# Optimization experiments

Measured on AMD Instinct MI355X. Metric: run time of the kernel, lower is better.

## Reference

```python
import jax, jax.numpy as jnp
import numpy as np

N_NODES = 100000
N_EDGES = 1600000
IN_F = 128
HEADS = 4
D_K = 32
OUT_TOTAL = HEADS * D_K


def setup_inputs() -> dict:
    key = jax.random.key(0)
    k1, k2, k3, k4, k5, k6 = jax.random.split(key, 6)
    x = jax.random.normal(k1, (N_NODES, IN_F), dtype=jnp.float32)
    edge_index = jax.random.randint(k2, (2, N_EDGES), 0, N_NODES, dtype=jnp.int64)
    # torch nn.Linear weights: [out, in], xavier-uniform init
    def xavier(k, shape):
        fan_out, fan_in = shape
        lim = float(np.sqrt(6.0 / (fan_in + fan_out)))
        return jax.random.uniform(k, shape, dtype=jnp.float32, minval=-lim, maxval=lim)
    Wq = xavier(k3, (OUT_TOTAL, IN_F))
    Wk = xavier(k4, (OUT_TOTAL, IN_F))
    Wv = xavier(k5, (OUT_TOTAL, IN_F))
    # D init_type='uniform': U(-1, 1)
    D = jax.random.uniform(k6, (HEADS, D_K), dtype=jnp.float32, minval=-1.0, maxval=1.0)
    return {"x": x, "Wq": Wq, "Wk": Wk, "Wv": Wv, "D": D, "edge_index": edge_index}


def reference(x, Wq, Wk, Wv, D, edge_index):
    N = x.shape[0]
    scale = 1.0 / np.sqrt(D_K)
    Q = (x @ Wq.T).reshape(N, HEADS, D_K)
    K = (x @ Wk.T).reshape(N, HEADS, D_K)
    V = (x @ Wv.T).reshape(N, HEADS, D_K)
    row, col = edge_index[0], edge_index[1]
    K_i = K[row]              # [E, H, d]
    Q_j = Q[col]              # [E, H, d]
    diff = K_i - Q_j
    # non-self edges: diff^T diag(D) diff ; self edges: K^T diag(D) Q
    score_edge = jnp.sum(diff * D * diff, axis=-1)          # [E, H]
    score_self = jnp.sum(K_i * D * Q[row], axis=-1)         # [E, H]
    self_mask = (row == col)[:, None]
    scores = jnp.where(self_mask, score_self, score_edge)
    scores = jax.nn.leaky_relu(scores * scale, 0.2)
    # segment softmax over destination node `row`
    smax = jax.ops.segment_max(scores, row, num_segments=N)  # [N, H]
    ex = jnp.exp(scores - smax[row])
    ssum = jax.ops.segment_sum(ex, row, num_segments=N)      # [N, H]
    alpha = ex / (ssum[row] + 1e-16)
    # scatter-add aggregate alpha * V[col] into destination rows
    out = jax.ops.segment_sum(alpha[:, :, None] * V[col], row, num_segments=N)
    return out.reshape(N, OUT_TOTAL)
```

## Files before the change

### kernel.cpp

```cpp
#include <hip/hip_runtime.h>
#include <hip/hip_fp16.h>
#include <cmath>


#define HEADS 4
#define DK 32
#define FDIM 128
#define BINSHIFT 8
#define BINCAP 6144

typedef _Float16 f16x8 __attribute__((ext_vector_type(8)));
typedef float f32x4 __attribute__((ext_vector_type(4)));

__global__ __launch_bounds__(256) void split_w(
    const float* __restrict__ Wq, const float* __restrict__ Wk,
    const float* __restrict__ Wv, _Float16* __restrict__ Whf,
    _Float16* __restrict__ Wlf, int* __restrict__ bin_cursor, int nb)
{
    const int gid = blockIdx.x * 256 + threadIdx.x;
    if (gid < nb) bin_cursor[gid] = 0;

    const int p = blockIdx.x;
    const float* __restrict__ W = (p == 0) ? Wq : (p == 1 ? Wk : Wv);
#pragma unroll
    for (int i = 0; i < 8; ++i) {
        const int id = i * 256 + threadIdx.x;
        const int g  = id >> 8;
        const int kc = (id >> 6) & 3;
        const int l  = id & 63;
        const int row  = g * 16 + (l & 15);
        const int col0 = kc * 32 + (l >> 4) * 8;
        const float* src = W + row * FDIM + col0;
        const float4 v0 = *reinterpret_cast<const float4*>(src);
        const float4 v1 = *reinterpret_cast<const float4*>(src + 4);
        const float vv[8] = {v0.x, v0.y, v0.z, v0.w, v1.x, v1.y, v1.z, v1.w};
        f16x8 h, lo;
#pragma unroll
        for (int j = 0; j < 8; ++j) {
            _Float16 hh = (_Float16)vv[j];
            h[j]  = hh;
            lo[j] = (_Float16)(vv[j] - (float)hh);
        }
        const size_t off = ((size_t)((p * 8 + g) * 4 + kc) * 64 + l) * 8;
        *reinterpret_cast<f16x8*>(Whf + off) = h;
        *reinterpret_cast<f16x8*>(Wlf + off) = lo;
    }
}

__global__ __launch_bounds__(256) void partition_edges(
    const int* __restrict__ row, const int* __restrict__ col,
    int* __restrict__ bin_cursor, unsigned* __restrict__ pairs,
    int E, int N, int NB)
{
    __shared__ int hist[512];
    __shared__ int basea[512];
    __shared__ int cura[512];
    const int tid = threadIdx.x;
    for (int b = tid; b < 512; b += 256) { hist[b] = 0; cura[b] = 0; }
    __syncthreads();

    const int e0 = blockIdx.x * 4096;
    int rr[16], cc[16];
    if (e0 + 4096 <= E) {
#pragma unroll
        for (int i = 0; i < 4; ++i) {
            const int idx = e0 + i * 1024 + tid * 4;
            const int4 r4 = *reinterpret_cast<const int4*>(row + idx);
            const int4 c4 = *reinterpret_cast<const int4*>(col + idx);
            rr[i*4+0] = r4.x; rr[i*4+1] = r4.y; rr[i*4+2] = r4.z; rr[i*4+3] = r4.w;
            cc[i*4+0] = c4.x; cc[i*4+1] = c4.y; cc[i*4+2] = c4.z; cc[i*4+3] = c4.w;
        }
    } else {
#pragma unroll
        for (int i = 0; i < 4; ++i)
#pragma unroll
            for (int j = 0; j < 4; ++j) {
                const int idx = e0 + i * 1024 + tid * 4 + j;
                rr[i*4+j] = (idx < E) ? row[idx] : -1;
                cc[i*4+j] = (idx < E) ? col[idx] : 0;
            }
    }

#pragma unroll
    for (int i = 0; i < 16; ++i)
        if ((unsigned)rr[i] < (unsigned)N)
            atomicAdd(&hist[rr[i] >> BINSHIFT], 1);
    __syncthreads();

    for (int b = tid; b < NB; b += 256) {
        const int h = hist[b];
        basea[b] = h ? atomicAdd(&bin_cursor[b], h) : 0;
    }
    __syncthreads();

#pragma unroll
    for (int i = 0; i < 16; ++i) {
        const int r = rr[i];
        if ((unsigned)r < (unsigned)N) {
            const int b = r >> BINSHIFT;
            const int p = basea[b] + atomicAdd(&cura[b], 1);
            if (p < BINCAP)
                pairs[(size_t)b * BINCAP + p] =
                    (unsigned)(r & 255) | ((unsigned)cc[i] << 8);
        }
    }
}

__global__ __launch_bounds__(256) void build_csr(
    const int* __restrict__ bin_cursor, const unsigned* __restrict__ pairs,
    int* __restrict__ csr, int* __restrict__ offA, int* __restrict__ cntA,
    int N)
{
    __shared__ int deg[256];
    __shared__ int offs[256];
    __shared__ int cur[256];
    const int b = blockIdx.x;
    const int tid = threadIdx.x;
    deg[tid] = 0;
    __syncthreads();

    int nsize = bin_cursor[b];
    if (nsize > BINCAP) nsize = BINCAP;
    const unsigned* bp = pairs + (size_t)b * BINCAP;

    for (int i = tid; i < nsize; i += 256)
        atomicAdd(&deg[bp[i] & 255], 1);
    __syncthreads();

    const int v = deg[tid];
    offs[tid] = v;
    __syncthreads();
    for (int o = 1; o < 256; o <<= 1) {
        const int t = (tid >= o) ? offs[tid - o] : 0;
        __syncthreads();
        offs[tid] += t;
        __syncthreads();
    }
    const int excl = offs[tid] - v;
    cur[tid] = excl;
    const int node = (b << BINSHIFT) + tid;
    if (node < N) {
        offA[node] = b * BINCAP + excl;
        cntA[node] = v;
    }
    __syncthreads();

    for (int i = tid; i < nsize; i += 256) {
        const unsigned pv = bp[i];
        const int p = atomicAdd(&cur[pv & 255], 1);
        csr[(size_t)b * BINCAP + p] = (int)((pv >> 8) << 9);
    }
}

__device__ __forceinline__ int swz_idx(int row, int kk) {
    return (row * FDIM + kk) ^ ((row & 7) << 3);
}

__device__ __forceinline__ void stage_x(
    const float* __restrict__ src, _Float16* __restrict__ dh,
    _Float16* __restrict__ dl, int n0, int nmax, int tid)
{
    const int kk0 = (tid & 15) * 8;
    const int r0  = tid >> 4;
#pragma unroll
    for (int i = 0; i < 4; ++i) {
        const int row = i * 16 + r0;
        float4 v0 = make_float4(0.f, 0.f, 0.f, 0.f), v1 = v0;
        if (n0 + row < nmax) {
            const float* p = src + (size_t)(n0 + row) * FDIM + kk0;
            v0 = *reinterpret_cast<const float4*>(p);
            v1 = *reinterpret_cast<const float4*>(p + 4);
        }
        const float vv[8] = {v0.x, v0.y, v0.z, v0.w, v1.x, v1.y, v1.z, v1.w};
        f16x8 h, l;
#pragma unroll
        for (int j = 0; j < 8; ++j) {
            _Float16 hh = (_Float16)vv[j];
            h[j] = hh;
            l[j] = (_Float16)(vv[j] - (float)hh);
        }
        const int si = swz_idx(row, kk0);
        *reinterpret_cast<f16x8*>(&dh[si]) = h;
        *reinterpret_cast<f16x8*>(&dl[si]) = l;
    }
}

__global__ __launch_bounds__(256) void qkv_gemm(
    const float* __restrict__ x, const _Float16* __restrict__ Whf,
    const _Float16* __restrict__ Wlf, __half* __restrict__ QVh,
    float* __restrict__ Kout, int N)
{
    __shared__ __align__(16) _Float16 xh[64 * 128];
    __shared__ __align__(16) _Float16 xl[64 * 128];

    const int n0  = blockIdx.x * 64;
    const int tid = threadIdx.x;
    const int lane = tid & 63;
    const int wv   = tid >> 6;
    const int wr0  = (wv >> 1) * 32;
    const int wc0  = (wv & 1) * 64;
    const int g0   = wc0 >> 4;
    const int orow = (lane >> 4) * 4;
    const int ocol = lane & 15;

    stage_x(x, xh, xl, n0, N, tid);
    __syncthreads();

    const int lrow = lane & 15;
    const int lk   = (lane >> 4) * 8;

    for (int p = 0; p < 3; ++p) {
        f32x4 acc[2][4];
#pragma unroll
        for (int a = 0; a < 2; ++a)
#pragma unroll
            for (int b = 0; b < 4; ++b)
                acc[a][b] = (f32x4){0.f, 0.f, 0.f, 0.f};

#pragma unroll
        for (int kc = 0; kc < 4; ++kc) {
            f16x8 afh[2], afl[2], bfh[4], bfl[4];
#pragma unroll
            for (int a = 0; a < 2; ++a) {
                const int si = swz_idx(wr0 + a * 16 + lrow, kc * 32 + lk);
                afh[a] = *reinterpret_cast<const f16x8*>(&xh[si]);
                afl[a] = *reinterpret_cast<const f16x8*>(&xl[si]);
            }
#pragma unroll
            for (int b = 0; b < 4; ++b) {
                const size_t off =
                    ((size_t)((p * 8 + g0 + b) * 4 + kc) * 64 + lane) * 8;
                bfh[b] = *reinterpret_cast<const f16x8*>(Whf + off);
                bfl[b] = *reinterpret_cast<const f16x8*>(Wlf + off);
            }
#pragma unroll
            for (int a = 0; a < 2; ++a)
#pragma unroll
                for (int b = 0; b < 4; ++b)
                    acc[a][b] = __builtin_amdgcn_mfma_f32_16x16x32_f16(
                        afh[a], bfh[b], acc[a][b], 0, 0, 0);
#pragma unroll
            for (int a = 0; a < 2; ++a)
#pragma unroll
                for (int b = 0; b < 4; ++b)
                    acc[a][b] = __builtin_amdgcn_mfma_f32_16x16x32_f16(
                        afl[a], bfh[b], acc[a][b], 0, 0, 0);
#pragma unroll
            for (int a = 0; a < 2; ++a)
#pragma unroll
                for (int b = 0; b < 4; ++b)
                    acc[a][b] = __builtin_amdgcn_mfma_f32_16x16x32_f16(
                        afh[a], bfl[b], acc[a][b], 0, 0, 0);
        }

        if (p == 1) {
#pragma unroll
            for (int a = 0; a < 2; ++a) {
#pragma unroll
                for (int r = 0; r < 4; ++r) {
                    const int n = n0 + wr0 + a * 16 + orow + r;
                    if (n < N) {
                        float* op = Kout + (size_t)n * FDIM + wc0 + ocol;
#pragma unroll
                        for (int b = 0; b < 4; ++b)
                            op[b * 16] = acc[a][b][r];
                    }
                }
            }
        } else {
            const int voff = (p == 2) ? 4 : 0;
#pragma unroll
            for (int a = 0; a < 2; ++a) {
#pragma unroll
                for (int r = 0; r < 4; ++r) {
                    const int n = n0 + wr0 + a * 16 + orow + r;
                    if (n < N) {
                        __half* op = QVh + (size_t)n * 256;
#pragma unroll
                        for (int b = 0; b < 4; ++b) {
                            const int d_o = wc0 + ocol + b * 16;
                            op[((d_o >> 2) << 3) + (d_o & 3) + voff] =
                                __float2half(acc[a][b][r]);
                        }
                    }
                }
            }
        }
    }
}

__global__ __launch_bounds__(256) void fused_aggregate(
    const int* __restrict__ offA, const int* __restrict__ cntA,
    const int* __restrict__ csr, const __half* __restrict__ QVh,
    const float* Kb, const float* __restrict__ D, float* out, int N)
{
    int node = blockIdx.x * 4 + (threadIdx.x >> 6);
    if (node >= N) return;
    const int lane = threadIdx.x & 63;
    const int hl   = lane & 31;
    const int side = lane >> 5;
    const int d0   = hl << 2;
    const float4 kv = *reinterpret_cast<const float4*>(Kb + (size_t)node * FDIM + d0);
    const float4 Dv = *reinterpret_cast<const float4*>(D + d0);
    const float Dk0 = Dv.x * kv.x, Dk1 = Dv.y * kv.y,
                Dk2 = Dv.z * kv.z, Dk3 = Dv.w * kv.w;
    const int j0  = offA[node];
    const int cnt = cntA[node];
    const int nb  = node << 9;
    float a0 = 0.f, a1 = 0.f, a2 = 0.f, a3 = 0.f, se = 0.f;

    int cc0, cc1, cc2, cc3;
    float4 t0, t1, t2, t3;

#define LOADP(s, p) { int c_ = __shfl(ecb, 2 * (p) + side); cc##s = c_; \
    t##s = *reinterpret_cast<const float4*>( \
        reinterpret_cast<const char*>(QVh) + (size_t)(unsigned)c_ + (hl << 4)); }

#define PROCP(s) { \
    const __half2* th = reinterpret_cast<const __half2*>(&t##s); \
    float2 q01 = __half22float2(th[0]); float2 q23 = __half22float2(th[1]); \
    float2 v01 = __half22float2(th[2]); float2 v23 = __half22float2(th[3]); \
    float p; \
    if (cc##s == nb) { \
        p = Dk0 * q01.x + Dk1 * q01.y + Dk2 * q23.x + Dk3 * q23.y; \
    } else { \
        float e0 = kv.x - q01.x, e1 = kv.y - q01.y; \
        float e2 = kv.z - q23.x, e3 = kv.w - q23.y; \
        p = Dv.x*e0*e0 + Dv.y*e1*e1 + Dv.z*e2*e2 + Dv.w*e3*e3; \
    } \
    p += __shfl_xor(p, 1); p += __shfl_xor(p, 2); p += __shfl_xor(p, 4); \
    float z = p * 0.17677669529663687f; \
    z = fmaxf(z, 0.2f * z); \
    float ex = __expf(z); \
    a0 += ex * v01.x; a1 += ex * v01.y; \
    a2 += ex * v23.x; a3 += ex * v23.y; se += ex; }

    for (int base = 0; base < cnt; base += 64) {
        const int rem = min(64, cnt - base);
        const int ecb = (lane < rem) ? csr[j0 + base + lane] : 0;
        const int npair = rem >> 1;
        int pj = 0;
        if (npair >= 4) {
            LOADP(0, 0) LOADP(1, 1) LOADP(2, 2) LOADP(3, 3)
            while (pj + 8 <= npair) {
                PROCP(0) LOADP(0, pj + 4)
                PROCP(1) LOADP(1, pj + 5)
                PROCP(2) LOADP(2, pj + 6)
                PROCP(3) LOADP(3, pj + 7)
                pj += 4;
            }
            PROCP(0) PROCP(1) PROCP(2) PROCP(3)
            pj += 4;
        }
        for (; pj < npair; ++pj) {
            LOADP(0, pj)
            PROCP(0)
        }
        if (rem & 1) {
            const int c_ = __shfl(ecb, rem - 1);
            float4 tt = *reinterpret_cast<const float4*>(
                reinterpret_cast<const char*>(QVh) + (size_t)(unsigned)c_ + (hl << 4));
            const __half2* th = reinterpret_cast<const __half2*>(&tt);
            float2 q01 = __half22float2(th[0]); float2 q23 = __half22float2(th[1]);
            float2 v01 = __half22float2(th[2]); float2 v23 = __half22float2(th[3]);
            float p;
            if (c_ == nb) {
                p = Dk0 * q01.x + Dk1 * q01.y + Dk2 * q23.x + Dk3 * q23.y;
            } else {
                float e0 = kv.x - q01.x, e1 = kv.y - q01.y;
                float e2 = kv.z - q23.x, e3 = kv.w - q23.y;
                p = Dv.x*e0*e0 + Dv.y*e1*e1 + Dv.z*e2*e2 + Dv.w*e3*e3;
            }
            p += __shfl_xor(p, 1); p += __shfl_xor(p, 2); p += __shfl_xor(p, 4);
            float z = p * 0.17677669529663687f;
            z = fmaxf(z, 0.2f * z);
            float ex = __expf(z) * 0.5f;
            a0 += ex * v01.x; a1 += ex * v01.y;
            a2 += ex * v23.x; a3 += ex * v23.y; se += ex;
        }
    }
#undef LOADP
#undef PROCP

    a0 += __shfl_xor(a0, 32); a1 += __shfl_xor(a1, 32);
    a2 += __shfl_xor(a2, 32); a3 += __shfl_xor(a3, 32);
    se += __shfl_xor(se, 32);

    if (side == 0) {
        const float inv = 1.0f / (se + 1e-16f);
        *reinterpret_cast<float4*>(out + (size_t)node * FDIM + d0) =
            make_float4(a0 * inv, a1 * inv, a2 * inv, a3 * inv);
    }
}

extern "C" void kernel_launch(void* const* d_in, const int* in_sizes, int n_in,
                              void* d_out, int out_size, void* d_ws, size_t ws_size,
                              hipStream_t stream) {
    const float* x  = (const float*)d_in[0];
    const float* Wq = (const float*)d_in[1];
    const float* Wk = (const float*)d_in[2];
    const float* Wv = (const float*)d_in[3];
    const float* D  = (const float*)d_in[4];
    const int*  edge = (const int*)d_in[5];
    float* out = (float*)d_out;

    const int N = in_sizes[0] / FDIM;
    const int E = in_sizes[5] / 2;
    const int* row = edge;
    const int* col = edge + E;

    const int NB = (N + 255) >> 8;

    __half* QVh = (__half*)d_ws;
    unsigned* pairs = (unsigned*)(QVh + (size_t)N * 256);
    int* csr  = (int*)(pairs + (size_t)NB * BINCAP);
    int* offA = csr + (size_t)NB * BINCAP;
    int* cntA = offA + N;
    int* bin_cursor = cntA + N;
    _Float16* Whf = (_Float16*)(bin_cursor + 512);
    _Float16* Wlf = Whf + 3 * 16384;
    float* Kout = out;

    split_w<<<3, 256, 0, stream>>>(Wq, Wk, Wv, Whf, Wlf, bin_cursor, NB);

    partition_edges<<<(E + 4095) / 4096, 256, 0, stream>>>(
        row, col, bin_cursor, pairs, E, N, NB);
    build_csr<<<NB, 256, 0, stream>>>(
        bin_cursor, pairs, csr, offA, cntA, N);

    qkv_gemm<<<(N + 63) / 64, 256, 0, stream>>>(
        x, Whf, Wlf, QVh, Kout, N);

    fused_aggregate<<<(N + 3) / 4, 256, 0, stream>>>(
        offA, cntA, csr, QVh, Kout, D, out, N);
}
```

Before: 313.2 us.

## Merge QKV GEMM and edge partitioning into one heterogeneous launch

Combines the edge-partition kernel and the QKV projection GEMM into a single launch whose blocks are interleaved by index. Some blocks bin edges into per-node-bucket pair lists and the rest run the fp16-split MFMA GEMM, sharing one 32KB shared buffer. The aim is to overlap the atomic-heavy, memory-bound partition work with the compute-bound GEMM and to drop one kernel launch and its tail. In exchange every block reserves the larger shared-memory footprint, which can lower occupancy for the partition blocks, and block-type selection adds a division per block.

```diff
diff --git a/kernel.cpp b/kernel.cpp
--- a/kernel.cpp
+++ b/kernel.cpp
@@ -47,61 +47,205 @@
     }
 }
 
-__global__ __launch_bounds__(256) void partition_edges(
+__device__ __forceinline__ int swz_idx(int row, int kk) {
+    return (row * FDIM + kk) ^ ((row & 7) << 3);
+}
+
+__device__ __forceinline__ void stage_x(
+    const float* __restrict__ src, _Float16* __restrict__ dh,
+    _Float16* __restrict__ dl, int n0, int nmax, int tid)
+{
+    const int kk0 = (tid & 15) * 8;
+    const int r0  = tid >> 4;
+#pragma unroll
+    for (int i = 0; i < 4; ++i) {
+        const int row = i * 16 + r0;
+        float4 v0 = make_float4(0.f, 0.f, 0.f, 0.f), v1 = v0;
+        if (n0 + row < nmax) {
+            const float* p = src + (size_t)(n0 + row) * FDIM + kk0;
+            v0 = *reinterpret_cast<const float4*>(p);
+            v1 = *reinterpret_cast<const float4*>(p + 4);
+        }
+        const float vv[8] = {v0.x, v0.y, v0.z, v0.w, v1.x, v1.y, v1.z, v1.w};
+        f16x8 h, l;
+#pragma unroll
+        for (int j = 0; j < 8; ++j) {
+            _Float16 hh = (_Float16)vv[j];
+            h[j] = hh;
+            l[j] = (_Float16)(vv[j] - (float)hh);
+        }
+        const int si = swz_idx(row, kk0);
+        *reinterpret_cast<f16x8*>(&dh[si]) = h;
+        *reinterpret_cast<f16x8*>(&dl[si]) = l;
+    }
+}
+
+__global__ __launch_bounds__(256) void qkv_and_partition(
+    const float* __restrict__ x, const _Float16* __restrict__ Whf,
+    const _Float16* __restrict__ Wlf, __half* __restrict__ QVh,
+    float* __restrict__ Kout, int N, int NQ, int NF,
     const int* __restrict__ row, const int* __restrict__ col,
-    int* __restrict__ bin_cursor, unsigned* __restrict__ pairs,
-    int E, int N, int NB)
+    int* __restrict__ bin_cursor, unsigned* __restrict__ pairs, int E, int NB)
 {
-    __shared__ int hist[512];
-    __shared__ int basea[512];
-    __shared__ int cura[512];
+    __shared__ __align__(16) char smem[32768];
+
+    const long T = (long)NQ + NF;
+    const long bid = blockIdx.x;
+    const int fprev = (int)((bid * NF) / T);
+    const int fcur  = (int)(((bid + 1) * NF) / T);
+
+    if (fcur > fprev) {
+        int* hist  = (int*)smem;
+        int* basea = hist + 512;
+        int* cura  = basea + 512;
+        const int tid = threadIdx.x;
+        for (int b = tid; b < 512; b += 256) { hist[b] = 0; cura[b] = 0; }
+        __syncthreads();
+
+        const int e0 = fprev * 4096;
+        int rr[16], cc[16];
+        if (e0 + 4096 <= E) {
+#pragma unroll
+            for (int i = 0; i < 4; ++i) {
+                const int idx = e0 + i * 1024 + tid * 4;
+                const int4 r4 = *reinterpret_cast<const int4*>(row + idx);
+                const int4 c4 = *reinterpret_cast<const int4*>(col + idx);
+                rr[i*4+0] = r4.x; rr[i*4+1] = r4.y; rr[i*4+2] = r4.z; rr[i*4+3] = r4.w;
+                cc[i*4+0] = c4.x; cc[i*4+1] = c4.y; cc[i*4+2] = c4.z; cc[i*4+3] = c4.w;
+            }
+        } else {
+#pragma unroll
+            for (int i = 0; i < 4; ++i)
+#pragma unroll
+                for (int j = 0; j < 4; ++j) {
+                    const int idx = e0 + i * 1024 + tid * 4 + j;
+                    rr[i*4+j] = (idx < E) ? row[idx] : -1;
+                    cc[i*4+j] = (idx < E) ? col[idx] : 0;
+                }
+        }
+
+#pragma unroll
+        for (int i = 0; i < 16; ++i)
+            if ((unsigned)rr[i] < (unsigned)N)
+                atomicAdd(&hist[rr[i] >> BINSHIFT], 1);
+        __syncthreads();
+
+        for (int b = tid; b < NB; b += 256) {
+            const int h = hist[b];
+            basea[b] = h ? atomicAdd(&bin_cursor[b], h) : 0;
+        }
+        __syncthreads();
+
+#pragma unroll
+        for (int i = 0; i < 16; ++i) {
+            const int r = rr[i];
+            if ((unsigned)r < (unsigned)N) {
+                const int b = r >> BINSHIFT;
+                const int p = basea[b] + atomicAdd(&cura[b], 1);
+                if (p < BINCAP)
+                    pairs[(size_t)b * BINCAP + p] =
+                        (unsigned)(r & 255) | ((unsigned)cc[i] << 8);
+            }
+        }
+        return;
+    }
+
+    _Float16* xh = (_Float16*)smem;
+    _Float16* xl = (_Float16*)(smem + 16384);
+
+    const int qidx = (int)bid - fprev;
+    const int n0  = qidx * 64;
     const int tid = threadIdx.x;
-    for (int b = tid; b < 512; b += 256) { hist[b] = 0; cura[b] = 0; }
+    const int lane = tid & 63;
+    const int wv   = tid >> 6;
+    const int wr0  = (wv >> 1) * 32;
+    const int wc0  = (wv & 1) * 64;
+    const int g0   = wc0 >> 4;
+    const int orow = (lane >> 4) * 4;
+    const int ocol = lane & 15;
+
+    stage_x(x, xh, xl, n0, N, tid);
     __syncthreads();
 
-    const int e0 = blockIdx.x * 4096;
-    int rr[16], cc[16];
-    if (e0 + 4096 <= E) {
-#pragma unroll
-        for (int i = 0; i < 4; ++i) {
-            const int idx = e0 + i * 1024 + tid * 4;
-            const int4 r4 = *reinterpret_cast<const int4*>(row + idx);
-            const int4 c4 = *reinterpret_cast<const int4*>(col + idx);
-            rr[i*4+0] = r4.x; rr[i*4+1] = r4.y; rr[i*4+2] = r4.z; rr[i*4+3] = r4.w;
-            cc[i*4+0] = c4.x; cc[i*4+1] = c4.y; cc[i*4+2] = c4.z; cc[i*4+3] = c4.w;
-        }
-    } else {
-#pragma unroll
-        for (int i = 0; i < 4; ++i)
-#pragma unroll
-            for (int j = 0; j < 4; ++j) {
-                const int idx = e0 + i * 1024 + tid * 4 + j;
-                rr[i*4+j] = (idx < E) ? row[idx] : -1;
-                cc[i*4+j] = (idx < E) ? col[idx] : 0;
-            }
-    }
-
-#pragma unroll
-    for (int i = 0; i < 16; ++i)
-        if ((unsigned)rr[i] < (unsigned)N)
-            atomicAdd(&hist[rr[i] >> BINSHIFT], 1);
-    __syncthreads();
-
-    for (int b = tid; b < NB; b += 256) {
-        const int h = hist[b];
-        basea[b] = h ? atomicAdd(&bin_cursor[b], h) : 0;
-    }
-    __syncthreads();
-
-#pragma unroll
-    for (int i = 0; i < 16; ++i) {
-        const int r = rr[i];
-        if ((unsigned)r < (unsigned)N) {
-            const int b = r >> BINSHIFT;
-            const int p = basea[b] + atomicAdd(&cura[b], 1);
-            if (p < BINCAP)
-                pairs[(size_t)b * BINCAP + p] =
-                    (unsigned)(r & 255) | ((unsigned)cc[i] << 8);
+    const int lrow = lane & 15;
+    const int lk   = (lane >> 4) * 8;
+
+    for (int p = 0; p < 3; ++p) {
+        f32x4 acc[2][4];
+#pragma unroll
+        for (int a = 0; a < 2; ++a)
+#pragma unroll
+            for (int b = 0; b < 4; ++b)
+                acc[a][b] = (f32x4){0.f, 0.f, 0.f, 0.f};
+
+#pragma unroll
+        for (int kc = 0; kc < 4; ++kc) {
+            f16x8 afh[2], afl[2], bfh[4], bfl[4];
+#pragma unroll
+            for (int a = 0; a < 2; ++a) {
+                const int si = swz_idx(wr0 + a * 16 + lrow, kc * 32 + lk);
+                afh[a] = *reinterpret_cast<const f16x8*>(&xh[si]);
+                afl[a] = *reinterpret_cast<const f16x8*>(&xl[si]);
+            }
+#pragma unroll
+            for (int b = 0; b < 4; ++b) {
+                const size_t off =
+                    ((size_t)((p * 8 + g0 + b) * 4 + kc) * 64 + lane) * 8;
+                bfh[b] = *reinterpret_cast<const f16x8*>(Whf + off);
+                bfl[b] = *reinterpret_cast<const f16x8*>(Wlf + off);
+            }
+#pragma unroll
+            for (int a = 0; a < 2; ++a)
+#pragma unroll
+                for (int b = 0; b < 4; ++b)
+                    acc[a][b] = __builtin_amdgcn_mfma_f32_16x16x32_f16(
+                        afh[a], bfh[b], acc[a][b], 0, 0, 0);
+#pragma unroll
+            for (int a = 0; a < 2; ++a)
+#pragma unroll
+                for (int b = 0; b < 4; ++b)
+                    acc[a][b] = __builtin_amdgcn_mfma_f32_16x16x32_f16(
+                        afl[a], bfh[b], acc[a][b], 0, 0, 0);
+#pragma unroll
+            for (int a = 0; a < 2; ++a)
+#pragma unroll
+                for (int b = 0; b < 4; ++b)
+                    acc[a][b] = __builtin_amdgcn_mfma_f32_16x16x32_f16(
+                        afh[a], bfl[b], acc[a][b], 0, 0, 0);
+        }
+
+        if (p == 1) {
+#pragma unroll
+            for (int a = 0; a < 2; ++a) {
+#pragma unroll
+                for (int r = 0; r < 4; ++r) {
+                    const int n = n0 + wr0 + a * 16 + orow + r;
+                    if (n < N) {
+                        float* op = Kout + (size_t)n * FDIM + wc0 + ocol;
+#pragma unroll
+                        for (int b = 0; b < 4; ++b)
+                            op[b * 16] = acc[a][b][r];
+                    }
+                }
+            }
+        } else {
+            const int voff = (p == 2) ? 4 : 0;
+#pragma unroll
+            for (int a = 0; a < 2; ++a) {
+#pragma unroll
+                for (int r = 0; r < 4; ++r) {
+                    const int n = n0 + wr0 + a * 16 + orow + r;
+                    if (n < N) {
+                        __half* op = QVh + (size_t)n * 256;
+#pragma unroll
+                        for (int b = 0; b < 4; ++b) {
+                            const int d_o = wc0 + ocol + b * 16;
+                            op[((d_o >> 2) << 3) + (d_o & 3) + voff] =
+                                __float2half(acc[a][b][r]);
+                        }
+                    }
+                }
+            }
         }
     }
 }
@@ -149,143 +293,6 @@
         const unsigned pv = bp[i];
         const int p = atomicAdd(&cur[pv & 255], 1);
         csr[(size_t)b * BINCAP + p] = (int)((pv >> 8) << 9);
-    }
-}
-
-__device__ __forceinline__ int swz_idx(int row, int kk) {
-    return (row * FDIM + kk) ^ ((row & 7) << 3);
-}
-
-__device__ __forceinline__ void stage_x(
-    const float* __restrict__ src, _Float16* __restrict__ dh,
-    _Float16* __restrict__ dl, int n0, int nmax, int tid)
-{
-    const int kk0 = (tid & 15) * 8;
-    const int r0  = tid >> 4;
-#pragma unroll
-    for (int i = 0; i < 4; ++i) {
-        const int row = i * 16 + r0;
-        float4 v0 = make_float4(0.f, 0.f, 0.f, 0.f), v1 = v0;
-        if (n0 + row < nmax) {
-            const float* p = src + (size_t)(n0 + row) * FDIM + kk0;
-            v0 = *reinterpret_cast<const float4*>(p);
-            v1 = *reinterpret_cast<const float4*>(p + 4);
-        }
-        const float vv[8] = {v0.x, v0.y, v0.z, v0.w, v1.x, v1.y, v1.z, v1.w};
-        f16x8 h, l;
-#pragma unroll
-        for (int j = 0; j < 8; ++j) {
-            _Float16 hh = (_Float16)vv[j];
-            h[j] = hh;
-            l[j] = (_Float16)(vv[j] - (float)hh);
-        }
-        const int si = swz_idx(row, kk0);
-        *reinterpret_cast<f16x8*>(&dh[si]) = h;
-        *reinterpret_cast<f16x8*>(&dl[si]) = l;
-    }
-}
-
-__global__ __launch_bounds__(256) void qkv_gemm(
-    const float* __restrict__ x, const _Float16* __restrict__ Whf,
-    const _Float16* __restrict__ Wlf, __half* __restrict__ QVh,
-    float* __restrict__ Kout, int N)
-{
-    __shared__ __align__(16) _Float16 xh[64 * 128];
-    __shared__ __align__(16) _Float16 xl[64 * 128];
-
-    const int n0  = blockIdx.x * 64;
-    const int tid = threadIdx.x;
-    const int lane = tid & 63;
-    const int wv   = tid >> 6;
-    const int wr0  = (wv >> 1) * 32;
-    const int wc0  = (wv & 1) * 64;
-    const int g0   = wc0 >> 4;
-    const int orow = (lane >> 4) * 4;
-    const int ocol = lane & 15;
-
-    stage_x(x, xh, xl, n0, N, tid);
-    __syncthreads();
-
-    const int lrow = lane & 15;
-    const int lk   = (lane >> 4) * 8;
-
-    for (int p = 0; p < 3; ++p) {
-        f32x4 acc[2][4];
-#pragma unroll
-        for (int a = 0; a < 2; ++a)
-#pragma unroll
-            for (int b = 0; b < 4; ++b)
-                acc[a][b] = (f32x4){0.f, 0.f, 0.f, 0.f};
-
-#pragma unroll
-        for (int kc = 0; kc < 4; ++kc) {
-            f16x8 afh[2], afl[2], bfh[4], bfl[4];
-#pragma unroll
-            for (int a = 0; a < 2; ++a) {
-                const int si = swz_idx(wr0 + a * 16 + lrow, kc * 32 + lk);
-                afh[a] = *reinterpret_cast<const f16x8*>(&xh[si]);
-                afl[a] = *reinterpret_cast<const f16x8*>(&xl[si]);
-            }
-#pragma unroll
-            for (int b = 0; b < 4; ++b) {
-                const size_t off =
-                    ((size_t)((p * 8 + g0 + b) * 4 + kc) * 64 + lane) * 8;
-                bfh[b] = *reinterpret_cast<const f16x8*>(Whf + off);
-                bfl[b] = *reinterpret_cast<const f16x8*>(Wlf + off);
-            }
-#pragma unroll
-            for (int a = 0; a < 2; ++a)
-#pragma unroll
-                for (int b = 0; b < 4; ++b)
-                    acc[a][b] = __builtin_amdgcn_mfma_f32_16x16x32_f16(
-                        afh[a], bfh[b], acc[a][b], 0, 0, 0);
-#pragma unroll
-            for (int a = 0; a < 2; ++a)
-#pragma unroll
-                for (int b = 0; b < 4; ++b)
-                    acc[a][b] = __builtin_amdgcn_mfma_f32_16x16x32_f16(
-                        afl[a], bfh[b], acc[a][b], 0, 0, 0);
-#pragma unroll
-            for (int a = 0; a < 2; ++a)
-#pragma unroll
-                for (int b = 0; b < 4; ++b)
-                    acc[a][b] = __builtin_amdgcn_mfma_f32_16x16x32_f16(
-                        afh[a], bfl[b], acc[a][b], 0, 0, 0);
-        }
-
-        if (p == 1) {
-#pragma unroll
-            for (int a = 0; a < 2; ++a) {
-#pragma unroll
-                for (int r = 0; r < 4; ++r) {
-                    const int n = n0 + wr0 + a * 16 + orow + r;
-                    if (n < N) {
-                        float* op = Kout + (size_t)n * FDIM + wc0 + ocol;
-#pragma unroll
-                        for (int b = 0; b < 4; ++b)
-                            op[b * 16] = acc[a][b][r];
-                    }
-                }
-            }
-        } else {
-            const int voff = (p == 2) ? 4 : 0;
-#pragma unroll
-            for (int a = 0; a < 2; ++a) {
-#pragma unroll
-                for (int r = 0; r < 4; ++r) {
-                    const int n = n0 + wr0 + a * 16 + orow + r;
-                    if (n < N) {
-                        __half* op = QVh + (size_t)n * 256;
-#pragma unroll
-                        for (int b = 0; b < 4; ++b) {
-                            const int d_o = wc0 + ocol + b * 16;
-                            op[((d_o >> 2) << 3) + (d_o & 3) + voff] =
-                                __float2half(acc[a][b][r]);
-                        }
-                    }
-                }
-            }
-        }
     }
 }
 
@@ -421,16 +428,17 @@
     _Float16* Wlf = Whf + 3 * 16384;
     float* Kout = out;
 
+    const int NQ = (N + 63) / 64;
+    const int NF = (E + 4095) / 4096;
+
     split_w<<<3, 256, 0, stream>>>(Wq, Wk, Wv, Whf, Wlf, bin_cursor, NB);
 
-    partition_edges<<<(E + 4095) / 4096, 256, 0, stream>>>(
-        row, col, bin_cursor, pairs, E, N, NB);
+    qkv_and_partition<<<NQ + NF, 256, 0, stream>>>(
+        x, Whf, Wlf, QVh, Kout, N, NQ, NF, row, col, bin_cursor, pairs, E, NB);
+
     build_csr<<<NB, 256, 0, stream>>>(
         bin_cursor, pairs, csr, offA, cntA, N);
 
-    qkv_gemm<<<(N + 63) / 64, 256, 0, stream>>>(
-        x, Whf, Wlf, QVh, Kout, N);
-
     fused_aggregate<<<(N + 3) / 4, 256, 0, stream>>>(
         offA, cntA, csr, QVh, Kout, D, out, N);
 }
```

Result: faster. 296.4 us (-5.3%).
